# Optimization experiments

Hardware: AMD Instinct MI355X
Metric: run time of the kernel (lower is better)

## Reference

```python
import jax, jax.numpy as jnp
import numpy as np

KERNEL = 4  # conv kernel == stride (non-overlapping patches)


def _conv(x, W, b):
    # x: [B, Cin, H, W], W: [Cout, Cin, k, k] (OIHW), stride == kernel, VALID padding
    y = jax.lax.conv_general_dilated(
        x, W, window_strides=(KERNEL, KERNEL), padding='VALID',
        dimension_numbers=('NCHW', 'OIHW', 'NCHW'))
    return y + b[None, :, None, None]


def setup_inputs() -> dict:
    key = jax.random.key(0)
    ks = jax.random.split(key, 7)
    B, Cin, H, Wd = 4, 64, 256, 256
    Cout = 128
    s = 0.05
    return {
        'x': jax.random.normal(ks[0], (B, Cin, H, Wd), dtype=jnp.float32),
        'Wq': jax.random.normal(ks[1], (Cout, Cin, KERNEL, KERNEL), dtype=jnp.float32) * s,
        'bq': jax.random.normal(ks[2], (Cout,), dtype=jnp.float32) * s,
        'Wk': jax.random.normal(ks[3], (Cout, Cin, KERNEL, KERNEL), dtype=jnp.float32) * s,
        'bk': jax.random.normal(ks[4], (Cout,), dtype=jnp.float32) * s,
        'Wv': jax.random.normal(ks[5], (Cout, Cin, KERNEL, KERNEL), dtype=jnp.float32) * s,
        'bv': jax.random.normal(ks[6], (Cout,), dtype=jnp.float32) * s,
    }


def reference(x, Wq, bq, Wk, bk, Wv, bv):
    B = x.shape[0]
    q = _conv(x, Wq, bq)              # [B, O, Hp, Wp]
    O, Hp, Wp = q.shape[1], q.shape[2], q.shape[3]
    N = Hp * Wp
    q = q.reshape(B, O, N)
    k = _conv(x, Wk, bk).reshape(B, O, N)
    v = _conv(x, Wv, bv).reshape(B, O, N)
    # scores[b, n, m] = sum_o q[b,o,n] * k[b,o,m]  (NO scaling, as in original)
    scores = jnp.einsum('bon,bom->bnm', q, k)
    attn = jax.nn.softmax(scores, axis=-1)        # [B, N, N]
    # attended^T: out[b, o, n] = sum_m attn[b,n,m] * v[b,o,m]
    out = jnp.einsum('bnm,bom->bon', attn, v)
    return out.reshape(B, O, Hp, Wp)
```

## Files before the change

### kernel.cpp

```cpp
#include <hip/hip_runtime.h>
#include <cstdint>
#include <cstddef>

#define NB 4
#define NP 4096
#define OD 128

typedef _Float16 h16;
typedef _Float16 h16x8 __attribute__((ext_vector_type(8)));
typedef _Float16 h16x4 __attribute__((ext_vector_type(4)));
typedef _Float16 h16x2 __attribute__((ext_vector_type(2)));
typedef float    f32x4 __attribute__((ext_vector_type(4)));

#define LOG2E 1.44269504f
#define RTH   12.0f

__device__ __forceinline__ float fexp2(float x) { return __builtin_amdgcn_exp2f(x); }
__device__ __forceinline__ h16x2 cvt_pk(float a, float b) {
    return __builtin_bit_cast(h16x2, __builtin_amdgcn_cvt_pkrtz(a, b));
}

__device__ __forceinline__ void async16(const void* g, void* l) {
    __builtin_amdgcn_global_load_lds(
        (const __attribute__((address_space(1))) void*)g,
        (__attribute__((address_space(3))) void*)l, 16, 0, 0);
}

__global__ __launch_bounds__(256) void wcvt(
    const float* __restrict__ Wq, const float* __restrict__ Wk,
    const float* __restrict__ Wv, h16* __restrict__ W16s)
{
    int g = blockIdx.x * 256 + threadIdx.x;
    int mat = g >> 14, r = g & 16383;
    int kc = r >> 9, q = r & 511, o = q >> 2, csw = q & 3;
    int c = csw ^ ((o >> 1) & 3);
    const float* W = (mat == 0) ? Wq : (mat == 1) ? Wk : Wv;
    const float* src = W + (size_t)o * 1024 + kc * 32 + 8 * c;
    f32x4 a = *(const f32x4*)src;
    f32x4 b = *(const f32x4*)(src + 4);
    h16x8 h = {(h16)a.x, (h16)a.y, (h16)a.z, (h16)a.w,
               (h16)b.x, (h16)b.y, (h16)b.z, (h16)b.w};
    *(h16x8*)&W16s[(size_t)g * 8] = h;
}

__global__ __launch_bounds__(256, 2) void conv_qkv(
    const float* __restrict__ x, const h16* __restrict__ W16s,
    const float* __restrict__ bq, const float* __restrict__ bk,
    const float* __restrict__ bv,
    h16* __restrict__ qt, h16* __restrict__ kt, h16* __restrict__ vt)
{
    const int nt = blockIdx.x;
    const int b  = blockIdx.y;
    const int tid = threadIdx.x, lane = tid & 63, wv = tid >> 6;
    const int lr = lane & 15, qd = lane >> 4;
    const int o_w = 32 * wv;

    __shared__ __align__(16) char smem[85504];
    float* biasl = (float*)(smem + 83968);
    if (tid < 128) {
        biasl[tid] = bq[tid] * LOG2E;
        biasl[128 + tid] = bk[tid]; biasl[256 + tid] = bv[tid];
    }

    auto dmaW = [&](int kc, int bs) {
#pragma unroll
        for (int t = 0; t < 6; ++t) {
            int grp = wv * 6 + t;
            int mat = grp >> 3, sg = grp & 7;
            async16(W16s + ((size_t)(mat * 32 + kc) * 512 + sg * 64 + lane) * 8,
                    smem + bs * 24576 + mat * 8192 + sg * 1024);
        }
    };

    f32x4 xr[2][2];
    auto xload = [&](int kc, int sl) {
        int n = tid >> 2, kg = tid & 3;
        int c = kg >> 1, kh2 = (kg & 1) * 2;
        const float* p = &x[(((size_t)(b * 64 + 2 * kc + c) * 256) + 4 * nt + kh2) * 256 + 4 * n];
        xr[sl][0] = *(const f32x4*)p;
        xr[sl][1] = *(const f32x4*)(p + 256);
    };
    auto xwrite = [&](int sl, int xbs) {
        int n = tid >> 2, kg = tid & 3;
        int c = kg >> 1, kh2 = (kg & 1) * 2;
        h16x8 h = {(h16)xr[sl][0].x, (h16)xr[sl][0].y, (h16)xr[sl][0].z, (h16)xr[sl][0].w,
                   (h16)xr[sl][1].x, (h16)xr[sl][1].y, (h16)xr[sl][1].z, (h16)xr[sl][1].w};
        *(h16x8*)(smem + 73728 + xbs * 5120 + n * 80 + c * 32 + kh2 * 8) = h;
    };

    auto cbar = [&]() {
        asm volatile("s_waitcnt vmcnt(8) lgkmcnt(0)" ::: "memory");
        __builtin_amdgcn_s_barrier();
        __builtin_amdgcn_sched_barrier(0);
    };

    f32x4 acc[3][2][4];
#pragma unroll
    for (int m = 0; m < 3; ++m)
#pragma unroll
        for (int a = 0; a < 2; ++a)
#pragma unroll
            for (int c = 0; c < 4; ++c) acc[m][a][c] = (f32x4){0.f, 0.f, 0.f, 0.f};

    xload(0, 0); dmaW(0, 0);
    xload(1, 1); dmaW(1, 1);
    xwrite(0, 0);
    cbar();

    int wb = 0;
#pragma unroll 2
    for (int kc = 0; kc < 32; ++kc) {
        int xbs = kc & 1;
        if (kc + 2 < 32) {
            dmaW(kc + 2, (wb == 0) ? 2 : wb - 1);
            xload(kc + 2, xbs);
        }
        const h16* Xl = (const h16*)(smem + 73728 + xbs * 5120);
        const char* Wl = smem + wb * 24576;

        h16x8 bf[4];
#pragma unroll
        for (int tn = 0; tn < 4; ++tn)
            bf[tn] = *(const h16x8*)&Xl[(16 * tn + lr) * 40 + 8 * qd];
#pragma unroll
        for (int mat = 0; mat < 3; ++mat) {
            h16x8 af[2];
#pragma unroll
            for (int to = 0; to < 2; ++to) {
                int o = o_w + 16 * to + lr;
                af[to] = *(const h16x8*)(Wl + mat * 8192 + (size_t)(o * 4 + (qd ^ ((o >> 1) & 3))) * 16);
            }
#pragma unroll
            for (int to = 0; to < 2; ++to)
#pragma unroll
                for (int tn = 0; tn < 4; ++tn)
                    acc[mat][to][tn] = __builtin_amdgcn_mfma_f32_16x16x32_f16(af[to], bf[tn], acc[mat][to][tn], 0, 0, 0);
        }
        if (kc + 1 < 32) xwrite((kc + 1) & 1, 1 - xbs);
        wb = (wb == 2) ? 0 : wb + 1;
        if (kc < 30) cbar(); else __syncthreads();
    }

    const int n0 = nt * 64;
#pragma unroll
    for (int mat = 0; mat < 2; ++mat) {
        const float qs = (mat == 0) ? LOG2E : 1.0f;
        h16* bnc = (h16*)smem;
#pragma unroll
        for (int to = 0; to < 2; ++to)
#pragma unroll
            for (int tn = 0; tn < 4; ++tn) {
                int ob = o_w + 16 * to + 4 * qd;
                int n  = 16 * tn + lr;
                h16x4 hv = {(h16)(acc[mat][to][tn][0] * qs + biasl[mat * 128 + ob]),
                            (h16)(acc[mat][to][tn][1] * qs + biasl[mat * 128 + ob + 1]),
                            (h16)(acc[mat][to][tn][2] * qs + biasl[mat * 128 + ob + 2]),
                            (h16)(acc[mat][to][tn][3] * qs + biasl[mat * 128 + ob + 3])};
                *(h16x4*)&bnc[n * 136 + ob] = hv;
            }
        __syncthreads();
        h16* dst = mat ? kt : qt;
#pragma unroll
        for (int j = 0; j < 4; ++j) {
            int s = tid + 256 * j;
            int n = s >> 4, oc = s & 15;
            *(h16x8*)(dst + ((size_t)(b * NP + n0 + n)) * OD + 8 * oc) = *(h16x8*)&bnc[n * 136 + 8 * oc];
        }
        __syncthreads();
    }
    {
        h16* bnc = (h16*)smem;
#pragma unroll
        for (int to = 0; to < 2; ++to)
#pragma unroll
            for (int tn = 0; tn < 4; ++tn)
#pragma unroll
                for (int r = 0; r < 4; ++r) {
                    int o = o_w + 16 * to + 4 * qd + r;
                    int n = 16 * tn + lr;
                    bnc[o * 72 + n] = (h16)(acc[2][to][tn][r] + biasl[256 + o]);
                }
        __syncthreads();
#pragma unroll
        for (int j = 0; j < 4; ++j) {
            int s = tid + 256 * j;
            int o = s >> 3, ch = s & 7;
            int g = ch >> 2, q2 = ch & 3;
            h16x8 hv;
#pragma unroll
            for (int r2 = 0; r2 < 8; ++r2) {
                int mt = r2 >> 2, r = r2 & 3;
                hv[r2] = bnc[o * 72 + 32 * g + 16 * mt + 4 * q2 + r];
            }
            *(h16x8*)(vt + ((size_t)(b * OD + o)) * NP + n0 + 32 * g + 8 * q2) = hv;
        }
    }
}

template <int SP>
__global__ __launch_bounds__(256, 3) void flash_attn(
    const h16* __restrict__ qt, const h16* __restrict__ kt,
    const h16* __restrict__ vt, h16* __restrict__ po, float2* __restrict__ ml)
{
    constexpr int MR  = NP / SP;
    constexpr int NIT = MR / 32;
    const int nt = blockIdx.x, sp = blockIdx.y, b = blockIdx.z;
    const int tid = threadIdx.x, lane = tid & 63, wv = tid >> 6;
    const int lr = lane & 15, qd = lane >> 4;

    __shared__ __align__(16) char smem[49152];

    h16x8 qf[2][4];
#pragma unroll
    for (int rt = 0; rt < 2; ++rt)
#pragma unroll
        for (int kc = 0; kc < 4; ++kc)
            qf[rt][kc] = *(const h16x8*)&qt[((size_t)(b * NP + nt * 128 + 32 * wv + 16 * rt + lr)) * OD
                                            + 32 * kc + 8 * qd];

    float m_run[2] = {-1e30f, -1e30f};
    f32x4 lsum[2] = {(f32x4){0.f, 0.f, 0.f, 0.f}, (f32x4){0.f, 0.f, 0.f, 0.f}};
    f32x4 oacc[2][8];
#pragma unroll
    for (int rt = 0; rt < 2; ++rt)
#pragma unroll
        for (int t = 0; t < 8; ++t) oacc[rt][t] = (f32x4){0.f, 0.f, 0.f, 0.f};

    const h16* kp[2]; const h16* vp[2];
#pragma unroll
    for (int t = 0; t < 2; ++t) {
        int s = wv * 128 + t * 64 + lane;
        int m = s >> 4, ck = s & 15;
        kp[t] = kt + ((size_t)(b * NP + sp * MR + m)) * OD + 8 * (ck ^ (m & 15));
        int o = s >> 2, cv = s & 3;
        vp[t] = vt + ((size_t)(b * OD + o)) * NP + sp * MR + 8 * (cv ^ ((o >> 1) & 3));
    }
    const int ldw = wv * 2048;

    auto dma = [&](int bs) {
#pragma unroll
        for (int t = 0; t < 2; ++t) {
            async16(kp[t], smem + bs * 8192 + ldw + t * 1024);
            kp[t] += 32 * OD;
        }
#pragma unroll
        for (int t = 0; t < 2; ++t) {
            async16(vp[t], smem + 24576 + bs * 8192 + ldw + t * 1024);
            vp[t] += 32;
        }
    };

    asm volatile("s_waitcnt vmcnt(0)" ::: "memory");
    __builtin_amdgcn_sched_barrier(0);
    dma(0); dma(1);

    const h16x8 ones8 = {(h16)1.0f, (h16)1.0f, (h16)1.0f, (h16)1.0f,
                         (h16)1.0f, (h16)1.0f, (h16)1.0f, (h16)1.0f};

    int rb = 0, db = 2;
#pragma unroll 2
    for (int it = 0; it < NIT; ++it) {
        asm volatile("s_waitcnt lgkmcnt(0)" ::: "memory");
        __builtin_amdgcn_s_barrier();
        __builtin_amdgcn_sched_barrier(0);
        if (it + 2 < NIT) { dma(db); db = (db == 2) ? 0 : db + 1; }
        if (it + 2 < NIT)      asm volatile("s_waitcnt vmcnt(8)" ::: "memory");
        else if (it + 1 < NIT) asm volatile("s_waitcnt vmcnt(4)" ::: "memory");
        else                   asm volatile("s_waitcnt vmcnt(0)" ::: "memory");
        __builtin_amdgcn_s_barrier();
        __builtin_amdgcn_sched_barrier(0);

        const h16* Kb = (const h16*)(smem + rb * 8192);
        const h16* Vb = (const h16*)(smem + 24576 + rb * 8192);
        rb = (rb == 2) ? 0 : rb + 1;

        f32x4 sc[2][2];
#pragma unroll
        for (int rt = 0; rt < 2; ++rt)
#pragma unroll
            for (int mt = 0; mt < 2; ++mt) sc[rt][mt] = (f32x4){0.f, 0.f, 0.f, 0.f};
        __builtin_amdgcn_s_setprio(1);
#pragma unroll
        for (int mt = 0; mt < 2; ++mt)
#pragma unroll
            for (int kc = 0; kc < 4; ++kc) {
                h16x8 kf = *(const h16x8*)&Kb[(size_t)((16 * mt + lr) * 16 + ((4 * kc + qd) ^ lr)) * 8];
                sc[0][mt] = __builtin_amdgcn_mfma_f32_16x16x32_f16(kf, qf[0][kc], sc[0][mt], 0, 0, 0);
                sc[1][mt] = __builtin_amdgcn_mfma_f32_16x16x32_f16(kf, qf[1][kc], sc[1][mt], 0, 0, 0);
            }
        __builtin_amdgcn_s_setprio(0);

        float mxv[2];
#pragma unroll
        for (int rt = 0; rt < 2; ++rt) {
            float mx = fmaxf(fmaxf(fmaxf(sc[rt][0][0], sc[rt][0][1]), fmaxf(sc[rt][0][2], sc[rt][0][3])),
                             fmaxf(fmaxf(sc[rt][1][0], sc[rt][1][1]), fmaxf(sc[rt][1][2], sc[rt][1][3])));
            mx = fmaxf(mx, __shfl_xor(mx, 16));
            mxv[rt] = fmaxf(mx, __shfl_xor(mx, 32));
        }
        if (!__all((mxv[0] <= m_run[0] + RTH) & (mxv[1] <= m_run[1] + RTH))) {
#pragma unroll
            for (int rt = 0; rt < 2; ++rt) {
                float mn = fmaxf(m_run[rt], mxv[rt]);
                float al = fexp2(m_run[rt] - mn);
                m_run[rt] = mn;
#pragma unroll
                for (int r = 0; r < 4; ++r) lsum[rt][r] *= al;
#pragma unroll
                for (int to = 0; to < 8; ++to)
#pragma unroll
                    for (int r = 0; r < 4; ++r) oacc[rt][to][r] *= al;
            }
        }

        h16x8 pf8[2];
#pragma unroll
        for (int rt = 0; rt < 2; ++rt) {
            h16x2 pw[4];
#pragma unroll
            for (int mt = 0; mt < 2; ++mt)
#pragma unroll
                for (int rp = 0; rp < 2; ++rp) {
                    float e0 = fexp2(sc[rt][mt][2 * rp]     - m_run[rt]);
                    float e1 = fexp2(sc[rt][mt][2 * rp + 1] - m_run[rt]);
                    pw[2 * mt + rp] = cvt_pk(e0, e1);
                }
            pf8[rt] = (h16x8){pw[0][0], pw[0][1], pw[1][0], pw[1][1],
                              pw[2][0], pw[2][1], pw[3][0], pw[3][1]};
        }

        __builtin_amdgcn_s_setprio(1);
        lsum[0] = __builtin_amdgcn_mfma_f32_16x16x32_f16(ones8, pf8[0], lsum[0], 0, 0, 0);
        lsum[1] = __builtin_amdgcn_mfma_f32_16x16x32_f16(ones8, pf8[1], lsum[1], 0, 0, 0);
#pragma unroll
        for (int to = 0; to < 8; ++to) {
            int o = 16 * to + lr;
            h16x8 vv = *(const h16x8*)&Vb[(size_t)(o * 4 + (qd ^ ((o >> 1) & 3))) * 8];
#pragma unroll
            for (int rt = 0; rt < 2; ++rt)
                oacc[rt][to] = __builtin_amdgcn_mfma_f32_16x16x32_f16(vv, pf8[rt], oacc[rt][to], 0, 0, 0);
        }
        __builtin_amdgcn_s_setprio(0);
    }

    const size_t nbase = (size_t)(sp * NB + b) * NP + nt * 128 + 32 * wv;
    if (qd == 0) {
#pragma unroll
        for (int rt = 0; rt < 2; ++rt)
            ml[nbase + 16 * rt + lr] = make_float2(m_run[rt], lsum[rt][0]);
    }
    float inv[2] = {1.f / lsum[0][0], 1.f / lsum[1][0]};
#pragma unroll
    for (int rt = 0; rt < 2; ++rt)
#pragma unroll
        for (int to = 0; to < 8; ++to) {
            h16x4 hv = {(h16)(oacc[rt][to][0] * inv[rt]), (h16)(oacc[rt][to][1] * inv[rt]),
                        (h16)(oacc[rt][to][2] * inv[rt]), (h16)(oacc[rt][to][3] * inv[rt])};
            *(h16x4*)&po[(nbase + 16 * rt + lr) * OD + 16 * to + 4 * qd] = hv;
        }
}

template <int SP>
__global__ __launch_bounds__(256) void combine(
    const h16* __restrict__ po, const float2* __restrict__ ml,
    float* __restrict__ out)
{
    const int nt = blockIdx.x, b = blockIdx.y;
    const int n0 = nt * 32, tid = threadIdx.x;
    __shared__ float w[SP][32];
    __shared__ float bn[32 * 130];

    if (tid < 32) {
        int n = n0 + tid;
        float m[SP], l[SP], M = -1e30f;
#pragma unroll
        for (int s = 0; s < SP; ++s) {
            float2 v = ml[(size_t)(s * NB + b) * NP + n];
            m[s] = v.x; l[s] = v.y;
            M = fmaxf(M, m[s]);
        }
        float d = 0.f, e[SP];
#pragma unroll
        for (int s = 0; s < SP; ++s) { e[s] = l[s] * fexp2(m[s] - M); d += e[s]; }
        float id = 1.f / d;
#pragma unroll
        for (int s = 0; s < SP; ++s) w[s][tid] = e[s] * id;
    }
    __syncthreads();

#pragma unroll
    for (int j = 0; j < 2; ++j) {
        int s = tid + 256 * j;
        int n = s >> 4, oc = s & 15;
        float acc[8];
#pragma unroll
        for (int k = 0; k < 8; ++k) acc[k] = 0.f;
#pragma unroll
        for (int sp = 0; sp < SP; ++sp) {
            h16x8 v = *(const h16x8*)&po[((size_t)(sp * NB + b) * NP + n0 + n) * OD + 8 * oc];
            float ww = w[sp][n];
#pragma unroll
            for (int k = 0; k < 8; ++k) acc[k] += ww * (float)v[k];
        }
#pragma unroll
        for (int k = 0; k < 8; ++k) bn[n * 130 + 8 * oc + k] = acc[k];
    }
    __syncthreads();

#pragma unroll
    for (int j = 0; j < 4; ++j) {
        int s = tid + 256 * j;
        int o = s >> 3, n4 = s & 7;
        f32x4 r = {bn[(4 * n4 + 0) * 130 + o], bn[(4 * n4 + 1) * 130 + o],
                   bn[(4 * n4 + 2) * 130 + o], bn[(4 * n4 + 3) * 130 + o]};
        *(f32x4*)&out[((size_t)(b * OD + o)) * NP + n0 + 4 * n4] = r;
    }
}

extern "C" void kernel_launch(void* const* d_in, const int* in_sizes, int n_in,
                              void* d_out, int out_size, void* d_ws, size_t ws_size,
                              hipStream_t stream) {
    const float* x  = (const float*)d_in[0];
    const float* Wq = (const float*)d_in[1];
    const float* bq = (const float*)d_in[2];
    const float* Wk = (const float*)d_in[3];
    const float* bk = (const float*)d_in[4];
    const float* Wv = (const float*)d_in[5];
    const float* bv = (const float*)d_in[6];

    h16* qtp  = (h16*)d_ws;
    h16* ktp  = qtp + (size_t)NB * NP * OD;
    h16* vtp  = ktp + (size_t)NB * NP * OD;
    h16* W16s = vtp + (size_t)NB * NP * OD;
    h16* po   = W16s + (size_t)3 * 32 * 512 * 8;
    float* out = (float*)d_out;

    wcvt<<<dim3(192), 256, 0, stream>>>(Wq, Wk, Wv, W16s);
    conv_qkv<<<dim3(64, NB), 256, 0, stream>>>(x, W16s, bq, bk, bv, qtp, ktp, vtp);

    const size_t base = 13369344;
    const size_t need8 = base + (size_t)8 * NB * NP * OD * 2 + (size_t)8 * NB * NP * 8;
    if (ws_size >= need8) {
        float2* ml = (float2*)(po + (size_t)8 * NB * NP * OD);
        flash_attn<8><<<dim3(32, 8, NB), 256, 0, stream>>>(qtp, ktp, vtp, po, ml);
        combine<8><<<dim3(128, NB), 256, 0, stream>>>(po, ml, out);
    } else {
        float2* ml = (float2*)(po + (size_t)4 * NB * NP * OD);
        flash_attn<4><<<dim3(32, 4, NB), 256, 0, stream>>>(qtp, ktp, vtp, po, ml);
        combine<4><<<dim3(128, NB), 256, 0, stream>>>(po, ml, out);
    }
}
```

Before: 192.6 us.

## Split conv_qkv across 8 waves and merge flash-attn loop barriers into one

```diff
diff --git a/kernel.cpp b/kernel.cpp
--- a/kernel.cpp
+++ b/kernel.cpp
@@ -43,7 +43,7 @@
     *(h16x8*)&W16s[(size_t)g * 8] = h;
 }
 
-__global__ __launch_bounds__(256, 2) void conv_qkv(
+__global__ __launch_bounds__(512, 2) void conv_qkv(
     const float* __restrict__ x, const h16* __restrict__ W16s,
     const float* __restrict__ bq, const float* __restrict__ bk,
     const float* __restrict__ bv,
@@ -53,7 +53,8 @@
     const int b  = blockIdx.y;
     const int tid = threadIdx.x, lane = tid & 63, wv = tid >> 6;
     const int lr = lane & 15, qd = lane >> 4;
-    const int o_w = 32 * wv;
+    const int wo = wv & 3, wn = wv >> 2;
+    const int o_w = 32 * wo, n_w = 32 * wn;
 
     __shared__ __align__(16) char smem[85504];
     float* biasl = (float*)(smem + 83968);
@@ -64,43 +65,40 @@
 
     auto dmaW = [&](int kc, int bs) {
 #pragma unroll
-        for (int t = 0; t < 6; ++t) {
-            int grp = wv * 6 + t;
+        for (int t = 0; t < 3; ++t) {
+            int grp = wv * 3 + t;
             int mat = grp >> 3, sg = grp & 7;
             async16(W16s + ((size_t)(mat * 32 + kc) * 512 + sg * 64 + lane) * 8,
                     smem + bs * 24576 + mat * 8192 + sg * 1024);
         }
     };
 
-    f32x4 xr[2][2];
+    f32x4 xr[2];
     auto xload = [&](int kc, int sl) {
-        int n = tid >> 2, kg = tid & 3;
-        int c = kg >> 1, kh2 = (kg & 1) * 2;
-        const float* p = &x[(((size_t)(b * 64 + 2 * kc + c) * 256) + 4 * nt + kh2) * 256 + 4 * n];
-        xr[sl][0] = *(const f32x4*)p;
-        xr[sl][1] = *(const f32x4*)(p + 256);
+        int n = tid >> 3, kg = tid & 7;
+        int c = kg >> 2, kh = kg & 3;
+        xr[sl] = *(const f32x4*)&x[(((size_t)(b * 64 + 2 * kc + c) * 256) + 4 * nt + kh) * 256 + 4 * n];
     };
     auto xwrite = [&](int sl, int xbs) {
-        int n = tid >> 2, kg = tid & 3;
-        int c = kg >> 1, kh2 = (kg & 1) * 2;
-        h16x8 h = {(h16)xr[sl][0].x, (h16)xr[sl][0].y, (h16)xr[sl][0].z, (h16)xr[sl][0].w,
-                   (h16)xr[sl][1].x, (h16)xr[sl][1].y, (h16)xr[sl][1].z, (h16)xr[sl][1].w};
-        *(h16x8*)(smem + 73728 + xbs * 5120 + n * 80 + c * 32 + kh2 * 8) = h;
+        int n = tid >> 3, kg = tid & 7;
+        int c = kg >> 2, kh = kg & 3;
+        h16x4 h = {(h16)xr[sl].x, (h16)xr[sl].y, (h16)xr[sl].z, (h16)xr[sl].w};
+        *(h16x4*)(smem + 73728 + xbs * 5120 + n * 80 + c * 32 + kh * 8) = h;
     };
 
     auto cbar = [&]() {
-        asm volatile("s_waitcnt vmcnt(8) lgkmcnt(0)" ::: "memory");
+        asm volatile("s_waitcnt vmcnt(4) lgkmcnt(0)" ::: "memory");
         __builtin_amdgcn_s_barrier();
         __builtin_amdgcn_sched_barrier(0);
     };
 
-    f32x4 acc[3][2][4];
+    f32x4 acc[3][2][2];
 #pragma unroll
     for (int m = 0; m < 3; ++m)
 #pragma unroll
         for (int a = 0; a < 2; ++a)
 #pragma unroll
-            for (int c = 0; c < 4; ++c) acc[m][a][c] = (f32x4){0.f, 0.f, 0.f, 0.f};
+            for (int c = 0; c < 2; ++c) acc[m][a][c] = (f32x4){0.f, 0.f, 0.f, 0.f};
 
     xload(0, 0); dmaW(0, 0);
     xload(1, 1); dmaW(1, 1);
@@ -118,10 +116,10 @@
         const h16* Xl = (const h16*)(smem + 73728 + xbs * 5120);
         const char* Wl = smem + wb * 24576;
 
-        h16x8 bf[4];
-#pragma unroll
-        for (int tn = 0; tn < 4; ++tn)
-            bf[tn] = *(const h16x8*)&Xl[(16 * tn + lr) * 40 + 8 * qd];
+        h16x8 bf[2];
+#pragma unroll
+        for (int tn = 0; tn < 2; ++tn)
+            bf[tn] = *(const h16x8*)&Xl[(n_w + 16 * tn + lr) * 40 + 8 * qd];
 #pragma unroll
         for (int mat = 0; mat < 3; ++mat) {
             h16x8 af[2];
@@ -133,7 +131,7 @@
 #pragma unroll
             for (int to = 0; to < 2; ++to)
 #pragma unroll
-                for (int tn = 0; tn < 4; ++tn)
+                for (int tn = 0; tn < 2; ++tn)
                     acc[mat][to][tn] = __builtin_amdgcn_mfma_f32_16x16x32_f16(af[to], bf[tn], acc[mat][to][tn], 0, 0, 0);
         }
         if (kc + 1 < 32) xwrite((kc + 1) & 1, 1 - xbs);
@@ -149,9 +147,9 @@
 #pragma unroll
         for (int to = 0; to < 2; ++to)
 #pragma unroll
-            for (int tn = 0; tn < 4; ++tn) {
+            for (int tn = 0; tn < 2; ++tn) {
                 int ob = o_w + 16 * to + 4 * qd;
-                int n  = 16 * tn + lr;
+                int n  = n_w + 16 * tn + lr;
                 h16x4 hv = {(h16)(acc[mat][to][tn][0] * qs + biasl[mat * 128 + ob]),
                             (h16)(acc[mat][to][tn][1] * qs + biasl[mat * 128 + ob + 1]),
                             (h16)(acc[mat][to][tn][2] * qs + biasl[mat * 128 + ob + 2]),
@@ -161,8 +159,8 @@
         __syncthreads();
         h16* dst = mat ? kt : qt;
 #pragma unroll
-        for (int j = 0; j < 4; ++j) {
-            int s = tid + 256 * j;
+        for (int j = 0; j < 2; ++j) {
+            int s = tid + 512 * j;
             int n = s >> 4, oc = s & 15;
             *(h16x8*)(dst + ((size_t)(b * NP + n0 + n)) * OD + 8 * oc) = *(h16x8*)&bnc[n * 136 + 8 * oc];
         }
@@ -173,17 +171,17 @@
 #pragma unroll
         for (int to = 0; to < 2; ++to)
 #pragma unroll
-            for (int tn = 0; tn < 4; ++tn)
+            for (int tn = 0; tn < 2; ++tn)
 #pragma unroll
                 for (int r = 0; r < 4; ++r) {
                     int o = o_w + 16 * to + 4 * qd + r;
-                    int n = 16 * tn + lr;
+                    int n = n_w + 16 * tn + lr;
                     bnc[o * 72 + n] = (h16)(acc[2][to][tn][r] + biasl[256 + o]);
                 }
         __syncthreads();
 #pragma unroll
-        for (int j = 0; j < 4; ++j) {
-            int s = tid + 256 * j;
+        for (int j = 0; j < 2; ++j) {
+            int s = tid + 512 * j;
             int o = s >> 3, ch = s & 7;
             int g = ch >> 2, q2 = ch & 3;
             h16x8 hv;
@@ -260,15 +258,11 @@
     int rb = 0, db = 2;
 #pragma unroll 2
     for (int it = 0; it < NIT; ++it) {
-        asm volatile("s_waitcnt lgkmcnt(0)" ::: "memory");
+        if (it < NIT - 1) asm volatile("s_waitcnt vmcnt(4) lgkmcnt(0)" ::: "memory");
+        else              asm volatile("s_waitcnt vmcnt(0) lgkmcnt(0)" ::: "memory");
         __builtin_amdgcn_s_barrier();
         __builtin_amdgcn_sched_barrier(0);
         if (it + 2 < NIT) { dma(db); db = (db == 2) ? 0 : db + 1; }
-        if (it + 2 < NIT)      asm volatile("s_waitcnt vmcnt(8)" ::: "memory");
-        else if (it + 1 < NIT) asm volatile("s_waitcnt vmcnt(4)" ::: "memory");
-        else                   asm volatile("s_waitcnt vmcnt(0)" ::: "memory");
-        __builtin_amdgcn_s_barrier();
-        __builtin_amdgcn_sched_barrier(0);
 
         const h16* Kb = (const h16*)(smem + rb * 8192);
         const h16* Vb = (const h16*)(smem + 24576 + rb * 8192);
@@ -436,7 +430,7 @@
     float* out = (float*)d_out;
 
     wcvt<<<dim3(192), 256, 0, stream>>>(Wq, Wk, Wv, W16s);
-    conv_qkv<<<dim3(64, NB), 256, 0, stream>>>(x, W16s, bq, bk, bv, qtp, ktp, vtp);
+    conv_qkv<<<dim3(64, NB), 512, 0, stream>>>(x, W16s, bq, bk, bv, qtp, ktp, vtp);
 
     const size_t base = 13369344;
     const size_t need8 = base + (size_t)8 * NB * NP * OD * 2 + (size_t)8 * NB * NP * 8;
```

Result: faster. 188.6 us (-2.1%).
